# Performance work log

Measured on AMD Instinct MI355X. Metric: run time of the kernel, lower is better.

## Reference

```python
import jax, jax.numpy as jnp
import numpy as np

L, D, B, N, H = 18, 256, 2, 1024, 4
HD = D // H  # head dim = 64
NAMES = ['self', 'cross'] * 9
BN_EPS = 1e-5


def conv1d(x, W, b):
    # pointwise Conv1d: x [B, Cin, N], W [Cout, Cin], b [Cout]
    return jnp.einsum('oi,bin->bon', W, x) + b[None, :, None]


def setup_inputs() -> dict:
    key = jax.random.key(0)
    ks = jax.random.split(key, 20)
    r = lambda k, shp, s=0.02: jax.random.normal(k, shp, dtype=jnp.float32) * s
    inp = {
        'desc0': jax.random.normal(ks[0], (B, D, N), dtype=jnp.float32),
        'desc1': jax.random.normal(ks[1], (B, D, N), dtype=jnp.float32),
        # attention projections (q, k, v, merge), stacked over layers
        'Wq': r(ks[2], (L, D, D)), 'bq': r(ks[3], (L, D)),
        'Wk': r(ks[4], (L, D, D)), 'bk': r(ks[5], (L, D)),
        'Wv': r(ks[6], (L, D, D)), 'bv': r(ks[7], (L, D)),
        'Wm': r(ks[8], (L, D, D)), 'bm': r(ks[9], (L, D)),
        # MLP([2D, 2D, D]): conv1 + BN(eval) + relu + conv2
        'W1': r(ks[10], (L, 2 * D, 2 * D)), 'b1': r(ks[11], (L, 2 * D)),
        'gamma': 1.0 + r(ks[12], (L, 2 * D)), 'beta': r(ks[13], (L, 2 * D)),
        'mu': r(ks[14], (L, 2 * D), 0.1),
        'var': 0.5 + jax.random.uniform(ks[15], (L, 2 * D), dtype=jnp.float32),
        'W2': r(ks[16], (L, D, 2 * D)), 'b2': r(ks[17], (L, D)),
    }
    return inp


def reference(desc0, desc1, Wq, bq, Wk, bk, Wv, bv, Wm, bm,
              W1, b1, gamma, beta, mu, var, W2, b2):
    d0, d1 = desc0, desc1
    bs = d0.shape[0]
    out0, out1 = [], []
    for i, name in enumerate(NAMES):
        x = jnp.concatenate([d0, d1], axis=0)           # [2B, D, N]
        src = x if name == 'self' else jnp.concatenate([d1, d0], axis=0)
        # QKV projections, split D -> (head_dim, H) matching torch .view(B, dim, H, -1)
        q = conv1d(x, Wq[i], bq[i]).reshape(2 * bs, HD, H, N)
        k = conv1d(src, Wk[i], bk[i]).reshape(2 * bs, HD, H, N)
        v = conv1d(src, Wv[i], bv[i]).reshape(2 * bs, HD, H, N)
        scores = jnp.einsum('bdhn,bdhm->bhnm', q, k) / np.sqrt(HD).astype(np.float32)
        prob = jax.nn.softmax(scores, axis=-1)          # [2B, H, N, N]
        att = jnp.einsum('bhnm,bdhm->bdhn', prob, v).reshape(2 * bs, D, N)
        message = conv1d(att, Wm[i], bm[i])             # merge
        y = jnp.concatenate([x, message], axis=1)       # [2B, 2D, N]
        h = conv1d(y, W1[i], b1[i])
        h = gamma[i][None, :, None] * (h - mu[i][None, :, None]) \
            * jax.lax.rsqrt(var[i][None, :, None] + BN_EPS) + beta[i][None, :, None]
        h = jax.nn.relu(h)
        delta = conv1d(h, W2[i], b2[i])                 # [2B, D, N]
        d0 = d0 + delta[:bs]
        d1 = d1 + delta[bs:]
        if name == 'cross':
            out0.append(d0)
            out1.append(d1)
    # [2, n_cross, B, D, N]
    return jnp.stack([jnp.stack(out0), jnp.stack(out1)])
```

## Files before the change

kernel.cpp:

```cpp
#include <hip/hip_runtime.h>
#include <math.h>


typedef unsigned short u16;
typedef unsigned int u32;
typedef __attribute__((ext_vector_type(4))) unsigned int u32x4;
typedef __attribute__((ext_vector_type(2))) unsigned int u32x2;
typedef __attribute__((ext_vector_type(8))) short short8v;
typedef __attribute__((ext_vector_type(4))) float f32x4;

union AB { u32x4 q; u32x2 d[2]; short8v s; };

__device__ __forceinline__ u16 f2bf(float f) {
  u32 u = __builtin_bit_cast(u32, f);
  u32 r = u + 0x7fffu + ((u >> 16) & 1u);
  return (u16)(r >> 16);
}

typedef const __attribute__((address_space(1))) void gas_t;
typedef __attribute__((address_space(3))) void las_t;
__device__ __forceinline__ void gld16(const void* g, void* l) {
  __builtin_amdgcn_global_load_lds((gas_t*)g, (las_t*)l, 16, 0, 0);
}
template<int NN>
__device__ __forceinline__ void waitvm() {
  if constexpr (NN == 0) asm volatile("s_waitcnt vmcnt(0)" ::: "memory");
  else if constexpr (NN == 1) asm volatile("s_waitcnt vmcnt(1)" ::: "memory");
  else asm volatile("s_waitcnt vmcnt(2)" ::: "memory");
}

template<int SN, int NK>
__device__ __forceinline__ void mm16g(const u16* __restrict__ Ar,
                                      const u16* const (&Br)[SN], f32x4 (&acc)[SN]) {
#pragma unroll
  for (int s = 0; s < SN; ++s) acc[s] = (f32x4){0.f, 0.f, 0.f, 0.f};
  AB a[2], b[2][SN];
  a[0].q = *(const u32x4*)(Ar);
#pragma unroll
  for (int s = 0; s < SN; ++s) b[0][s].q = *(const u32x4*)(Br[s]);
#pragma unroll
  for (int kp = 0; kp < NK; ++kp) {
    const int cu = kp & 1, nx = cu ^ 1;
    if (kp + 1 < NK) {
      a[nx].q = *(const u32x4*)(Ar + (kp + 1) * 32);
#pragma unroll
      for (int s = 0; s < SN; ++s) b[nx][s].q = *(const u32x4*)(Br[s] + (kp + 1) * 32);
    }
#pragma unroll
    for (int s = 0; s < SN; ++s)
      acc[s] = __builtin_amdgcn_mfma_f32_16x16x32_bf16(a[cu].s, b[cu][s].s, acc[s], 0, 0, 0);
  }
}

template<int LDB, int SN, int NS, int D>
__device__ __forceinline__ void mmlds(const u16* __restrict__ W, char* __restrict__ Wb,
                                      const char* __restrict__ Alds, f32x4 (&acc)[SN],
                                      int w, int lane, int l4, int l15, int R) {
  constexpr int BUFB = SN * 16384;
  constexpr int NBUF = D + 1;
  const int xj = (lane & 3) ^ ((lane >> 2) & 3) ^ ((lane >> 4) & 3);
  const int swzr = ((l15 & 3) ^ ((l15 >> 2) & 3)) << 4;
  const u16* gs = W + (size_t)(16 * w + (lane >> 2)) * LDB + xj * 8;
  char* ldsu = Wb + 16 * w * 64;
#pragma unroll
  for (int s = 0; s < SN; ++s) acc[s] = (f32x4){0.f, 0.f, 0.f, 0.f};
#pragma unroll
  for (int d = 0; d < D; ++d) {
    const int sl = (R + d) & (NS - 1);
#pragma unroll
    for (int c = 0; c < SN; ++c)
      gld16(gs + (size_t)c * 256 * LDB + (size_t)sl * 32, ldsu + d * BUFB + c * 16384);
  }
#pragma unroll
  for (int i = 0; i < NS; ++i) {
    const int rem = NS - 1 - i;
    if (rem >= D - 1) waitvm<SN*(D - 1)>();
    else if (rem == 1) waitvm<SN>();
    else waitvm<0>();
    __builtin_amdgcn_s_barrier();
    asm volatile("" ::: "memory");
    const int s = (i + R) & (NS - 1);
    const char* rb = Wb + (i % NBUF) * BUFB;
    AB af;
    af.q = *(const u32x4*)(Alds + ((l15 * 1024 + s * 64 + l4 * 16) ^ ((l15 & 7) << 4)));
#pragma unroll
    for (int t = 0; t < SN; ++t) {
      const int col = (w * SN + t) * 16 + l15;
      AB bf;
      bf.q = *(const u32x4*)(rb + col * 64 + ((l4 << 4) ^ swzr));
      acc[t] = __builtin_amdgcn_mfma_f32_16x16x32_bf16(af.s, bf.s, acc[t], 0, 0, 0);
    }
    if (i + D < NS) {
      const int sl = (i + D + R) & (NS - 1);
#pragma unroll
      for (int c = 0; c < SN; ++c)
        gld16(gs + (size_t)c * 256 * LDB + (size_t)sl * 32,
              ldsu + ((i + D) % NBUF) * BUFB + c * 16384);
    }
  }
}

__global__ void k_setup(const float* __restrict__ Wq, const float* __restrict__ Wk,
                        const float* __restrict__ Wv, const float* __restrict__ Wm,
                        const float* __restrict__ W1, const float* __restrict__ W2,
                        const float* __restrict__ g, const float* __restrict__ be,
                        const float* __restrict__ mu, const float* __restrict__ va,
                        const float* __restrict__ b1, u16* __restrict__ wbf,
                        float* __restrict__ sc, float* __restrict__ sh) {
  int bid = blockIdx.x, tid = threadIdx.x;
  if (bid < 4608) {
    int which = bid / 1152, lb = bid - which * 1152;
    size_t i4 = ((size_t)lb * 256 + tid) * 4;
    int layer = (int)(i4 >> 16), rem = (int)(i4 & 65535);
    int row = rem >> 8, kk = rem & 255;
    const float* src = which == 0 ? Wq : which == 1 ? Wk : which == 2 ? Wv : Wm;
    f32x4 a = *(const f32x4*)(src + i4);
    u16* dl = wbf + (size_t)layer * 655360 + which * 65536;
    if (which < 3) {
      float s = (which == 0) ? 0.125f : 1.0f;
      int rp = ((row & 3) << 6) | (row >> 2);
      u32x2 pk;
      pk[0] = (u32)f2bf(a[0] * s) | ((u32)f2bf(a[1] * s) << 16);
      pk[1] = (u32)f2bf(a[2] * s) | ((u32)f2bf(a[3] * s) << 16);
      *(u32x2*)(dl + rp * 256 + kk) = pk;
    } else {
#pragma unroll
      for (int e = 0; e < 4; ++e) {
        int ci = kk + e, cp = ((ci & 3) << 6) | (ci >> 2);
        dl[row * 256 + cp] = f2bf(a[e]);
      }
    }
  } else if (bid < 9216) {
    int lb = bid - 4608;
    size_t i4 = ((size_t)lb * 256 + tid) * 4;
    int layer = (int)(i4 >> 18);
    size_t rem = i4 & 262143;
    f32x4 a = *(const f32x4*)(W1 + i4);
    u32x2 pk;
    pk[0] = (u32)f2bf(a[0]) | ((u32)f2bf(a[1]) << 16);
    pk[1] = (u32)f2bf(a[2]) | ((u32)f2bf(a[3]) << 16);
    *(u32x2*)(wbf + (size_t)layer * 655360 + 262144 + rem) = pk;
  } else if (bid < 11520) {
    int lb = bid - 9216;
    size_t i4 = ((size_t)lb * 256 + tid) * 4;
    int layer = (int)(i4 >> 17);
    size_t rem = i4 & 131071;
    f32x4 a = *(const f32x4*)(W2 + i4);
    u32x2 pk;
    pk[0] = (u32)f2bf(a[0]) | ((u32)f2bf(a[1]) << 16);
    pk[1] = (u32)f2bf(a[2]) | ((u32)f2bf(a[3]) << 16);
    *(u32x2*)(wbf + (size_t)layer * 655360 + 524288 + rem) = pk;
  } else {
    int i = (bid - 11520) * 256 + tid;
    if (i < 9216) {
      float s = g[i] * rsqrtf(va[i] + 1e-5f);
      sc[i] = s;
      sh[i] = s * (b1[i] - mu[i]) + be[i];
    }
  }
}

__global__ __launch_bounds__(256) void k_init(const float* __restrict__ d0,
                                              const float* __restrict__ d1,
                                              float* __restrict__ dstate,
                                              u16* __restrict__ y) {
  __shared__ float T[64 * 65];
  int b = blockIdx.z, cb = blockIdx.y * 64, nb = blockIdx.x * 64;
  int t = threadIdx.x, th = t >> 4, tl = t & 15;
  const float* src = (b < 2 ? d0 : d1) + (size_t)(b & 1) * 262144;
#pragma unroll
  for (int it = 0; it < 4; ++it) {
    int cl = it * 16 + th;
    f32x4 v = *(const f32x4*)(src + (size_t)(cb + cl) * 1024 + nb + tl * 4);
#pragma unroll
    for (int e = 0; e < 4; ++e) T[cl * 65 + tl * 4 + e] = v[e];
  }
  __syncthreads();
#pragma unroll
  for (int it = 0; it < 4; ++it) {
    int nl = it * 16 + th;
    f32x4 o;
#pragma unroll
    for (int e = 0; e < 4; ++e) o[e] = T[(tl * 4 + e) * 65 + nl];
    *(f32x4*)(dstate + (size_t)b * 262144 + (size_t)(nb + nl) * 256 + cb + tl * 4) = o;
    u32x2 pk;
    pk[0] = (u32)f2bf(o[0]) | ((u32)f2bf(o[1]) << 16);
    pk[1] = (u32)f2bf(o[2]) | ((u32)f2bf(o[3]) << 16);
    *(u32x2*)(y + (size_t)b * 524288 + (size_t)(nb + nl) * 512 + cb + tl * 4) = pk;
  }
}

__global__ __launch_bounds__(512) void k_qkv0(const u16* __restrict__ y,
                                              const u16* __restrict__ wln,
                                              const float* __restrict__ bqn,
                                              const float* __restrict__ bkn,
                                              const float* __restrict__ bvn,
                                              u16* __restrict__ qb, u16* __restrict__ kb,
                                              u16* __restrict__ vb) {
  const int row0 = blockIdx.x * 16, b = row0 >> 10, nb0 = row0 & 1023;
  const int tid = threadIdx.x, w = tid >> 6, lane = tid & 63;
  const int l4 = lane >> 4, l15 = lane & 15;
  const u16* Ar = y + (size_t)(row0 + l15) * 512 + l4 * 8;
  const u16* Br[6];
  f32x4 acc[6];
  int ty[6], cc[6];
#pragma unroll
  for (int s = 0; s < 6; ++s) {
    int gc = w * 96 + s * 16;
    ty[s] = gc >> 8;
    cc[s] = gc & 255;
    Br[s] = wln + ty[s] * 65536 + (size_t)(cc[s] + l15) * 256 + l4 * 8;
  }
  mm16g<6, 8>(Ar, Br, acc);
#pragma unroll
  for (int s = 0; s < 6; ++s) {
    int c = cc[s] + l15;
    int borig = ((c & 63) << 2) | (c >> 6);
    if (ty[s] == 0) {
      float bb = 0.125f * bqn[borig];
#pragma unroll
      for (int r = 0; r < 4; ++r)
        qb[(size_t)b * 262144 + (size_t)(nb0 + l4 * 4 + r) * 256 + c] = f2bf(acc[s][r] + bb);
    } else if (ty[s] == 1) {
      float bb = bkn[borig];
#pragma unroll
      for (int r = 0; r < 4; ++r)
        kb[(size_t)b * 262144 + (size_t)(nb0 + l4 * 4 + r) * 256 + c] = f2bf(acc[s][r] + bb);
    } else {
      float bb = bvn[borig];
      u32x2 pk;
      pk[0] = (u32)f2bf(acc[s][0] + bb) | ((u32)f2bf(acc[s][1] + bb) << 16);
      pk[1] = (u32)f2bf(acc[s][2] + bb) | ((u32)f2bf(acc[s][3] + bb) << 16);
      *(u32x2*)(vb + (size_t)b * 262144 + (size_t)c * 1024 + nb0 + l4 * 4) = pk;
    }
  }
}

__global__ __launch_bounds__(512) void k_attn(const u16* __restrict__ qbuf,
                                              const u16* __restrict__ kbuf,
                                              const u16* __restrict__ vbuf,
                                              u16* __restrict__ att, int crossmask) {
  __shared__ char Kt[2][2][8192];
  __shared__ char Vt[2][2][8192];
  __shared__ char Ps[8][2304];
  __shared__ float Ms[4][16], Ls[4][16], Os[4][16][68];
  const int nb = blockIdx.x * 64;
  const int bh = blockIdx.y, b = bh >> 2, h = bh & 3;
  const int srcb = b ^ crossmask;
  const int tid = threadIdx.x, w = tid >> 6, lane = tid & 63;
  const int l4 = lane >> 4, l15 = lane & 15;
  const int qt = w & 3, half = w >> 2;
  char* P = Ps[w];
  const u16* Qb = qbuf + (size_t)b * 262144 + h * 64;
  const u16* Kb = kbuf + (size_t)srcb * 262144 + h * 64;
  const u16* Vb = vbuf + (size_t)srcb * 262144 + (size_t)h * 65536;
  const int srow = tid >> 3, sj = (tid & 7) * 16, sx = sj ^ ((srow & 7) << 4);
  const u16* gK[2] = {Kb, Kb + 512 * 256};
  const u16* gV[2] = {Vb, Vb + 512};

  const int qrow = nb + qt * 16;
  AB qf[2];
#pragma unroll
  for (int ks = 0; ks < 2; ++ks)
    qf[ks].q = *(const u32x4*)(Qb + (size_t)(qrow + l15) * 256 + ks * 32 + l4 * 8);

  u32x4 sk[2], sv[2];
#pragma unroll
  for (int H = 0; H < 2; ++H) {
    sk[H] = *(const u32x4*)((const char*)(gK[H] + (size_t)srow * 256) + sj);
    sv[H] = *(const u32x4*)((const char*)(gV[H] + (size_t)srow * 1024) + sj);
  }
#pragma unroll
  for (int H = 0; H < 2; ++H) {
    *(u32x4*)(Kt[H][0] + srow * 128 + sx) = sk[H];
    *(u32x4*)(Vt[H][0] + srow * 128 + sx) = sv[H];
  }
  __syncthreads();

  f32x4 oacc[4];
#pragma unroll
  for (int s = 0; s < 4; ++s) oacc[s] = (f32x4){0.f, 0.f, 0.f, 0.f};
  float mst = -1e30f, lst = 0.f;

#pragma unroll
  for (int mt = 0; mt < 8; ++mt) {
    const int cur = mt & 1, nx = cur ^ 1;
    if (mt < 7) {
#pragma unroll
      for (int H = 0; H < 2; ++H) {
        sk[H] = *(const u32x4*)((const char*)(gK[H] + (size_t)((mt + 1) * 64 + srow) * 256) + sj);
        sv[H] = *(const u32x4*)((const char*)(gV[H] + (size_t)srow * 1024 + (mt + 1) * 64) + sj);
      }
    }
    f32x4 sa[4];
#pragma unroll
    for (int sm = 0; sm < 4; ++sm) {
      sa[sm] = (f32x4){0.f, 0.f, 0.f, 0.f};
#pragma unroll
      for (int ks = 0; ks < 2; ++ks) {
        AB kf;
        int rr = sm * 16 + l15;
        kf.q = *(const u32x4*)(Kt[half][cur] + rr * 128 + ((ks * 64 + l4 * 16) ^ ((rr & 7) << 4)));
        sa[sm] = __builtin_amdgcn_mfma_f32_16x16x32_bf16(kf.s, qf[ks].s, sa[sm], 0, 0, 0);
      }
    }
    float m1 = fmaxf(fmaxf(fmaxf(sa[0][0], sa[0][1]), fmaxf(sa[0][2], sa[0][3])),
                     fmaxf(fmaxf(sa[1][0], sa[1][1]), fmaxf(sa[1][2], sa[1][3])));
    float m2 = fmaxf(fmaxf(fmaxf(sa[2][0], sa[2][1]), fmaxf(sa[2][2], sa[2][3])),
                     fmaxf(fmaxf(sa[3][0], sa[3][1]), fmaxf(sa[3][2], sa[3][3])));
    m1 = fmaxf(m1, m2);
    m1 = fmaxf(m1, __shfl_xor(m1, 16));
    m1 = fmaxf(m1, __shfl_xor(m1, 32));
    float mnew = fmaxf(mst, m1);
    float corr = __expf(mst - mnew);
    mst = mnew;
    float rs = 0.f;
#pragma unroll
    for (int sm = 0; sm < 4; ++sm)
#pragma unroll
      for (int r = 0; r < 4; ++r) {
        float p = __expf(sa[sm][r] - mnew);
        sa[sm][r] = p;
        rs += p;
      }
    rs += __shfl_xor(rs, 16);
    rs += __shfl_xor(rs, 32);
    lst = lst * corr + rs;
#pragma unroll
    for (int r = 0; r < 4; ++r) {
      float cr = __shfl(corr, l4 * 4 + r);
#pragma unroll
      for (int s = 0; s < 4; ++s) oacc[s][r] *= cr;
    }
#pragma unroll
    for (int sm = 0; sm < 4; ++sm) {
      u32x2 pk;
      pk[0] = (u32)f2bf(sa[sm][0]) | ((u32)f2bf(sa[sm][1]) << 16);
      pk[1] = (u32)f2bf(sa[sm][2]) | ((u32)f2bf(sa[sm][3]) << 16);
      *(u32x2*)(P + l15 * 136 + (sm * 16 + l4 * 4) * 2) = pk;
    }
#pragma unroll
    for (int ks = 0; ks < 2; ++ks) {
      AB pf;
      const char* ra = P + l15 * 136 + ks * 64 + l4 * 16;
      pf.d[0] = *(const u32x2*)ra;
      pf.d[1] = *(const u32x2*)(ra + 8);
#pragma unroll
      for (int s = 0; s < 4; ++s) {
        AB vf;
        int rr = s * 16 + l15;
        vf.q = *(const u32x4*)(Vt[half][cur] + rr * 128 + ((ks * 64 + l4 * 16) ^ ((rr & 7) << 4)));
        oacc[s] = __builtin_amdgcn_mfma_f32_16x16x32_bf16(pf.s, vf.s, oacc[s], 0, 0, 0);
      }
    }
    if (mt < 7) {
#pragma unroll
      for (int H = 0; H < 2; ++H) {
        *(u32x4*)(Kt[H][nx] + srow * 128 + sx) = sk[H];
        *(u32x4*)(Vt[H][nx] + srow * 128 + sx) = sv[H];
      }
    }
    __syncthreads();
  }
  if (half == 1) {
    Ms[qt][l15] = mst;
    Ls[qt][l15] = lst;
#pragma unroll
    for (int s = 0; s < 4; ++s)
#pragma unroll
      for (int r = 0; r < 4; ++r) Os[qt][l4 * 4 + r][s * 16 + l15] = oacc[s][r];
  }
  __syncthreads();
  if (half == 0) {
    float mb = Ms[qt][l15], lb = Ls[qt][l15];
    float M = fmaxf(mst, mb);
    float ea = __expf(mst - M), eb = __expf(mb - M);
    float rl = 1.f / (lst * ea + lb * eb);
    float fa = ea * rl, fb = eb * rl;
#pragma unroll
    for (int r = 0; r < 4; ++r) {
      float far = __shfl(fa, l4 * 4 + r);
      float fbr = __shfl(fb, l4 * 4 + r);
      int n = nb + qt * 16 + l4 * 4 + r;
#pragma unroll
      for (int s = 0; s < 4; ++s) {
        float ov = oacc[s][r] * far + Os[qt][l4 * 4 + r][s * 16 + l15] * fbr;
        att[(size_t)b * 262144 + (size_t)n * 256 + h * 64 + s * 16 + l15] = f2bf(ov);
      }
    }
  }
}

__global__ __launch_bounds__(1024) void k_post(
    const u16* __restrict__ att, const u16* __restrict__ wl, const u16* __restrict__ wln,
    const float* __restrict__ bm, const float* __restrict__ sc, const float* __restrict__ sh,
    const float* __restrict__ b2, const float* __restrict__ bqn,
    const float* __restrict__ bkn, const float* __restrict__ bvn,
    float* __restrict__ dstate, u16* __restrict__ y, u16* __restrict__ qb,
    u16* __restrict__ kb, u16* __restrict__ vb, float* __restrict__ out, int cross, int j,
    int last) {
  __shared__ char yT[16384];
  __shared__ char hT[16384];
  __shared__ char Wb[98304];
  const int bid = blockIdx.x;
  const int row0 = bid * 16, b = row0 >> 10, nb0 = row0 & 1023;
  const int tid = threadIdx.x, w = tid >> 6, lane = tid & 63;
  const int l4 = lane >> 4, l15 = lane & 15;

  {
    int rr = tid >> 6, ch = tid & 63;
    u32x4 v = *(const u32x4*)(y + (size_t)(row0 + rr) * 512 + ch * 8);
    *(u32x4*)(yT + ((rr * 1024 + ch * 16) ^ ((rr & 7) << 4))) = v;
    if (tid < 512) {
      int ra = tid >> 5, ca = tid & 31;
      u32x4 va = *(const u32x4*)(att + (size_t)(row0 + ra) * 256 + ca * 8);
      *(u32x4*)(hT + ((ra * 1024 + ca * 16) ^ ((ra & 7) << 4))) = va;
    }
  }
  __syncthreads();
  {
    f32x4 acc[1];
    mmlds<256, 1, 8, 3>(wl + 196608, Wb, hT, acc, w, lane, l4, l15, bid & 7);
    int c = w * 16 + l15;
    float bb = bm[c];
#pragma unroll
    for (int r = 0; r < 4; ++r) {
      int rw = l4 * 4 + r;
      *(u16*)(yT + ((rw * 1024 + (256 + c) * 2) ^ ((rw & 7) << 4))) = f2bf(acc[0][r] + bb);
    }
  }
  __syncthreads();
  {
    f32x4 acc[2];
    mmlds<512, 2, 16, 2>(wl + 262144, Wb, yT, acc, w, lane, l4, l15, bid & 15);
#pragma unroll
    for (int s = 0; s < 2; ++s) {
      int c = w * 32 + s * 16 + l15;
      float s_ = sc[c], t_ = sh[c];
#pragma unroll
      for (int r = 0; r < 4; ++r) {
        int rw = l4 * 4 + r;
        *(u16*)(hT + ((rw * 1024 + c * 2) ^ ((rw & 7) << 4))) =
            f2bf(fmaxf(s_ * acc[s][r] + t_, 0.f));
      }
    }
  }
  __syncthreads();
  {
    f32x4 acc[1];
    mmlds<512, 1, 16, 3>(wl + 524288, Wb, hT, acc, w, lane, l4, l15, bid & 15);
    float* ob = out + (size_t)(((b >> 1) * 9 + j) * 2 + (b & 1)) * 262144;
    int c = w * 16 + l15;
    float bb = b2[c];
#pragma unroll
    for (int r = 0; r < 4; ++r) {
      int rw = l4 * 4 + r;
      size_t di = (size_t)(row0 + rw) * 256 + c;
      float nv = dstate[di] + acc[0][r] + bb;
      dstate[di] = nv;
      u16 bv16 = f2bf(nv);
      y[(size_t)(row0 + rw) * 512 + c] = bv16;
      *(u16*)(yT + ((rw * 1024 + c * 2) ^ ((rw & 7) << 4))) = bv16;
      if (cross) ob[(size_t)c * 1024 + nb0 + rw] = nv;
    }
  }
  if (last) return;
  __syncthreads();
  {
    f32x4 acc[2];
    mmlds<256, 2, 8, 2>(wln, Wb, yT, acc, w, lane, l4, l15, bid & 7);
#pragma unroll
    for (int s = 0; s < 2; ++s) {
      int gc = w * 32 + s * 16;
      int ty = gc >> 8;
      int c = (gc & 255) + l15;
      int borig = ((c & 63) << 2) | (c >> 6);
      if (ty == 0) {
        float bb = 0.125f * bqn[borig];
#pragma unroll
        for (int r = 0; r < 4; ++r)
          qb[(size_t)b * 262144 + (size_t)(nb0 + l4 * 4 + r) * 256 + c] = f2bf(acc[s][r] + bb);
      } else {
        float bb = bkn[borig];
#pragma unroll
        for (int r = 0; r < 4; ++r)
          kb[(size_t)b * 262144 + (size_t)(nb0 + l4 * 4 + r) * 256 + c] = f2bf(acc[s][r] + bb);
      }
    }
  }
  __syncthreads();
  {
    f32x4 acc[1];
    mmlds<256, 1, 8, 3>(wln + 131072, Wb, yT, acc, w, lane, l4, l15, bid & 7);
    int c = w * 16 + l15;
    float bb = bvn[((c & 63) << 2) | (c >> 6)];
    u32x2 pk;
    pk[0] = (u32)f2bf(acc[0][0] + bb) | ((u32)f2bf(acc[0][1] + bb) << 16);
    pk[1] = (u32)f2bf(acc[0][2] + bb) | ((u32)f2bf(acc[0][3] + bb) << 16);
    *(u32x2*)(vb + (size_t)b * 262144 + (size_t)c * 1024 + nb0 + l4 * 4) = pk;
  }
}

extern "C" void kernel_launch(void* const* d_in, const int* in_sizes, int n_in,
                              void* d_out, int out_size, void* d_ws, size_t ws_size,
                              hipStream_t stream) {
  const float* desc0 = (const float*)d_in[0];
  const float* desc1 = (const float*)d_in[1];
  const float* Wq = (const float*)d_in[2];
  const float* bq = (const float*)d_in[3];
  const float* Wk = (const float*)d_in[4];
  const float* bk = (const float*)d_in[5];
  const float* Wv = (const float*)d_in[6];
  const float* bv = (const float*)d_in[7];
  const float* Wm = (const float*)d_in[8];
  const float* bm = (const float*)d_in[9];
  const float* W1 = (const float*)d_in[10];
  const float* b1 = (const float*)d_in[11];
  const float* gamma = (const float*)d_in[12];
  const float* beta = (const float*)d_in[13];
  const float* mu = (const float*)d_in[14];
  const float* var = (const float*)d_in[15];
  const float* W2 = (const float*)d_in[16];
  const float* b2 = (const float*)d_in[17];

  char* ws = (char*)d_ws;
  float* dstate = (float*)ws;
  u16* y = (u16*)(ws + ((size_t)4 << 20));
  u16* qb = (u16*)(ws + ((size_t)8 << 20));
  u16* kb = (u16*)(ws + ((size_t)10 << 20));
  u16* vb = (u16*)(ws + ((size_t)12 << 20));
  u16* attb = (u16*)(ws + ((size_t)14 << 20));
  u16* wbf = (u16*)(ws + ((size_t)16 << 20));
  float* scb = (float*)(ws + ((size_t)40 << 20));
  float* shb = (float*)(ws + ((size_t)41 << 20));

  k_setup<<<11556, 256, 0, stream>>>(Wq, Wk, Wv, Wm, W1, W2, gamma, beta, mu, var, b1,
                                     wbf, scb, shb);
  k_init<<<dim3(16, 4, 4), 256, 0, stream>>>(desc0, desc1, dstate, y);
  k_qkv0<<<256, 512, 0, stream>>>(y, wbf, bq, bk, bv, qb, kb, vb);

  for (int i = 0; i < 18; ++i) {
    int cross = i & 1;
    const u16* wl = wbf + (size_t)i * 655360;
    int nl = (i < 17) ? i + 1 : 0;
    const u16* wln = wbf + (size_t)nl * 655360;
    k_attn<<<dim3(16, 16), 512, 0, stream>>>(qb, kb, vb, attb, cross ? 2 : 0);
    k_post<<<256, 1024, 0, stream>>>(attb, wl, wln, bm + i * 256, scb + (size_t)i * 512,
                                     shb + (size_t)i * 512, b2 + i * 256, bq + nl * 256,
                                     bk + nl * 256, bv + nl * 256, dstate, y, qb, kb, vb,
                                     (float*)d_out, cross, i >> 1, i == 17);
  }
}
```

Before: 778.2 us.

## Double k_post row tile and give each wave a private weight ring

k_post now handles 32 rows per block instead of 16, with half as many blocks, so each weight slice streamed from global memory feeds two MFMA row groups. The shared, barrier-synchronised weight staging buffer is replaced by a per-wave three-slot ring, and each wave loads only its own 16-column slice, so the per-step block barriers go away. The cost is that only 128 blocks remain to occupy the GPU, and each wave now issues more sequential weight passes, which may expose load latency.

```diff
diff --git a/kernel.cpp b/kernel.cpp
--- a/kernel.cpp
+++ b/kernel.cpp
@@ -25,8 +25,7 @@
 template<int NN>
 __device__ __forceinline__ void waitvm() {
   if constexpr (NN == 0) asm volatile("s_waitcnt vmcnt(0)" ::: "memory");
-  else if constexpr (NN == 1) asm volatile("s_waitcnt vmcnt(1)" ::: "memory");
-  else asm volatile("s_waitcnt vmcnt(2)" ::: "memory");
+  else asm volatile("s_waitcnt vmcnt(1)" ::: "memory");
 }
 
 template<int SN, int NK>
@@ -52,50 +51,35 @@
   }
 }
 
-template<int LDB, int SN, int NS, int D>
-__device__ __forceinline__ void mmlds(const u16* __restrict__ W, char* __restrict__ Wb,
-                                      const char* __restrict__ Alds, f32x4 (&acc)[SN],
-                                      int w, int lane, int l4, int l15, int R) {
-  constexpr int BUFB = SN * 16384;
-  constexpr int NBUF = D + 1;
+template<int LDB, int NS>
+__device__ __forceinline__ void mmw(const u16* __restrict__ Wcol, char* __restrict__ ldsw,
+                                    const char* __restrict__ Alds, f32x4 (&acc)[2],
+                                    int lane, int l4, int l15, int R) {
   const int xj = (lane & 3) ^ ((lane >> 2) & 3) ^ ((lane >> 4) & 3);
   const int swzr = ((l15 & 3) ^ ((l15 >> 2) & 3)) << 4;
-  const u16* gs = W + (size_t)(16 * w + (lane >> 2)) * LDB + xj * 8;
-  char* ldsu = Wb + 16 * w * 64;
-#pragma unroll
-  for (int s = 0; s < SN; ++s) acc[s] = (f32x4){0.f, 0.f, 0.f, 0.f};
-#pragma unroll
-  for (int d = 0; d < D; ++d) {
+  const u16* gs = Wcol + (size_t)(lane >> 2) * LDB + xj * 8;
+  acc[0] = (f32x4){0.f, 0.f, 0.f, 0.f};
+  acc[1] = (f32x4){0.f, 0.f, 0.f, 0.f};
+#pragma unroll
+  for (int d = 0; d < 2; ++d) {
     const int sl = (R + d) & (NS - 1);
-#pragma unroll
-    for (int c = 0; c < SN; ++c)
-      gld16(gs + (size_t)c * 256 * LDB + (size_t)sl * 32, ldsu + d * BUFB + c * 16384);
+    gld16(gs + (size_t)sl * 32, ldsw + d * 1024);
   }
 #pragma unroll
   for (int i = 0; i < NS; ++i) {
-    const int rem = NS - 1 - i;
-    if (rem >= D - 1) waitvm<SN*(D - 1)>();
-    else if (rem == 1) waitvm<SN>();
+    if (i < NS - 1) waitvm<1>();
     else waitvm<0>();
-    __builtin_amdgcn_s_barrier();
-    asm volatile("" ::: "memory");
     const int s = (i + R) & (NS - 1);
-    const char* rb = Wb + (i % NBUF) * BUFB;
-    AB af;
-    af.q = *(const u32x4*)(Alds + ((l15 * 1024 + s * 64 + l4 * 16) ^ ((l15 & 7) << 4)));
-#pragma unroll
-    for (int t = 0; t < SN; ++t) {
-      const int col = (w * SN + t) * 16 + l15;
-      AB bf;
-      bf.q = *(const u32x4*)(rb + col * 64 + ((l4 << 4) ^ swzr));
-      acc[t] = __builtin_amdgcn_mfma_f32_16x16x32_bf16(af.s, bf.s, acc[t], 0, 0, 0);
-    }
-    if (i + D < NS) {
-      const int sl = (i + D + R) & (NS - 1);
-#pragma unroll
-      for (int c = 0; c < SN; ++c)
-        gld16(gs + (size_t)c * 256 * LDB + (size_t)sl * 32,
-              ldsu + ((i + D) % NBUF) * BUFB + c * 16384);
+    const char* rb = ldsw + (i % 3) * 1024;
+    AB af0, af1, bf;
+    af0.q = *(const u32x4*)(Alds + ((l15 * 1024 + s * 64 + l4 * 16) ^ ((l15 & 7) << 4)));
+    af1.q = *(const u32x4*)(Alds + (((16 + l15) * 1024 + s * 64 + l4 * 16) ^ ((l15 & 7) << 4)));
+    bf.q = *(const u32x4*)(rb + l15 * 64 + ((l4 << 4) ^ swzr));
+    acc[0] = __builtin_amdgcn_mfma_f32_16x16x32_bf16(af0.s, bf.s, acc[0], 0, 0, 0);
+    acc[1] = __builtin_amdgcn_mfma_f32_16x16x32_bf16(af1.s, bf.s, acc[1], 0, 0, 0);
+    if (i + 2 < NS) {
+      const int sl = (i + 2 + R) & (NS - 1);
+      gld16(gs + (size_t)sl * 32, ldsw + ((i + 2) % 3) * 1024);
     }
   }
 }
@@ -399,19 +383,24 @@
     float* __restrict__ dstate, u16* __restrict__ y, u16* __restrict__ qb,
     u16* __restrict__ kb, u16* __restrict__ vb, float* __restrict__ out, int cross, int j,
     int last) {
-  __shared__ char yT[16384];
-  __shared__ char hT[16384];
-  __shared__ char Wb[98304];
+  __shared__ char yT[32768];
+  __shared__ char hT[32768];
+  __shared__ char Wb[49152];
   const int bid = blockIdx.x;
-  const int row0 = bid * 16, b = row0 >> 10, nb0 = row0 & 1023;
+  const int row0 = bid * 32, b = row0 >> 10, nb0 = row0 & 1023;
   const int tid = threadIdx.x, w = tid >> 6, lane = tid & 63;
   const int l4 = lane >> 4, l15 = lane & 15;
+  char* ring = Wb + w * 3072;
 
   {
-    int rr = tid >> 6, ch = tid & 63;
-    u32x4 v = *(const u32x4*)(y + (size_t)(row0 + rr) * 512 + ch * 8);
-    *(u32x4*)(yT + ((rr * 1024 + ch * 16) ^ ((rr & 7) << 4))) = v;
-    if (tid < 512) {
+#pragma unroll
+    for (int it = 0; it < 2; ++it) {
+      int idx = it * 1024 + tid;
+      int rr = idx >> 6, ch = idx & 63;
+      u32x4 v = *(const u32x4*)(y + (size_t)(row0 + rr) * 512 + ch * 8);
+      *(u32x4*)(yT + ((rr * 1024 + ch * 16) ^ ((rr & 7) << 4))) = v;
+    }
+    {
       int ra = tid >> 5, ca = tid & 31;
       u32x4 va = *(const u32x4*)(att + (size_t)(row0 + ra) * 256 + ca * 8);
       *(u32x4*)(hT + ((ra * 1024 + ca * 16) ^ ((ra & 7) << 4))) = va;
@@ -419,85 +408,97 @@
   }
   __syncthreads();
   {
-    f32x4 acc[1];
-    mmlds<256, 1, 8, 3>(wl + 196608, Wb, hT, acc, w, lane, l4, l15, bid & 7);
+    f32x4 acc[2];
+    mmw<256, 8>(wl + 196608 + (size_t)(w * 16) * 256, ring, hT, acc, lane, l4, l15, bid & 7);
     int c = w * 16 + l15;
     float bb = bm[c];
 #pragma unroll
-    for (int r = 0; r < 4; ++r) {
-      int rw = l4 * 4 + r;
-      *(u16*)(yT + ((rw * 1024 + (256 + c) * 2) ^ ((rw & 7) << 4))) = f2bf(acc[0][r] + bb);
+    for (int g = 0; g < 2; ++g)
+#pragma unroll
+      for (int r = 0; r < 4; ++r) {
+        int rw = g * 16 + l4 * 4 + r;
+        *(u16*)(yT + ((rw * 1024 + (256 + c) * 2) ^ ((rw & 7) << 4))) = f2bf(acc[g][r] + bb);
+      }
+  }
+  __syncthreads();
+  {
+#pragma unroll
+    for (int p = 0; p < 2; ++p) {
+      f32x4 acc[2];
+      const int colbase = p * 256 + w * 16;
+      mmw<512, 16>(wl + 262144 + (size_t)colbase * 512, ring, yT, acc, lane, l4, l15,
+                   (bid + p * 5) & 15);
+      int c = colbase + l15;
+      float s_ = sc[c], t_ = sh[c];
+#pragma unroll
+      for (int g = 0; g < 2; ++g)
+#pragma unroll
+        for (int r = 0; r < 4; ++r) {
+          int rw = g * 16 + l4 * 4 + r;
+          *(u16*)(hT + ((rw * 1024 + c * 2) ^ ((rw & 7) << 4))) =
+              f2bf(fmaxf(s_ * acc[g][r] + t_, 0.f));
+        }
     }
   }
   __syncthreads();
   {
     f32x4 acc[2];
-    mmlds<512, 2, 16, 2>(wl + 262144, Wb, yT, acc, w, lane, l4, l15, bid & 15);
-#pragma unroll
-    for (int s = 0; s < 2; ++s) {
-      int c = w * 32 + s * 16 + l15;
-      float s_ = sc[c], t_ = sh[c];
-#pragma unroll
-      for (int r = 0; r < 4; ++r) {
-        int rw = l4 * 4 + r;
-        *(u16*)(hT + ((rw * 1024 + c * 2) ^ ((rw & 7) << 4))) =
-            f2bf(fmaxf(s_ * acc[s][r] + t_, 0.f));
-      }
-    }
-  }
-  __syncthreads();
-  {
-    f32x4 acc[1];
-    mmlds<512, 1, 16, 3>(wl + 524288, Wb, hT, acc, w, lane, l4, l15, bid & 15);
+    mmw<512, 16>(wl + 524288 + (size_t)(w * 16) * 512, ring, hT, acc, lane, l4, l15,
+                 bid & 15);
     float* ob = out + (size_t)(((b >> 1) * 9 + j) * 2 + (b & 1)) * 262144;
     int c = w * 16 + l15;
     float bb = b2[c];
 #pragma unroll
-    for (int r = 0; r < 4; ++r) {
-      int rw = l4 * 4 + r;
-      size_t di = (size_t)(row0 + rw) * 256 + c;
-      float nv = dstate[di] + acc[0][r] + bb;
-      dstate[di] = nv;
-      u16 bv16 = f2bf(nv);
-      y[(size_t)(row0 + rw) * 512 + c] = bv16;
-      *(u16*)(yT + ((rw * 1024 + c * 2) ^ ((rw & 7) << 4))) = bv16;
-      if (cross) ob[(size_t)c * 1024 + nb0 + rw] = nv;
-    }
+    for (int g = 0; g < 2; ++g)
+#pragma unroll
+      for (int r = 0; r < 4; ++r) {
+        int rw = g * 16 + l4 * 4 + r;
+        size_t di = (size_t)(row0 + rw) * 256 + c;
+        float nv = dstate[di] + acc[g][r] + bb;
+        dstate[di] = nv;
+        u16 bv16 = f2bf(nv);
+        y[(size_t)(row0 + rw) * 512 + c] = bv16;
+        *(u16*)(yT + ((rw * 1024 + c * 2) ^ ((rw & 7) << 4))) = bv16;
+        if (cross) ob[(size_t)c * 1024 + nb0 + rw] = nv;
+      }
   }
   if (last) return;
   __syncthreads();
   {
-    f32x4 acc[2];
-    mmlds<256, 2, 8, 2>(wln, Wb, yT, acc, w, lane, l4, l15, bid & 7);
-#pragma unroll
-    for (int s = 0; s < 2; ++s) {
-      int gc = w * 32 + s * 16;
-      int ty = gc >> 8;
-      int c = (gc & 255) + l15;
+#pragma unroll
+    for (int p = 0; p < 3; ++p) {
+      f32x4 acc[2];
+      mmw<256, 8>(wln + p * 65536 + (size_t)(w * 16) * 256, ring, yT, acc, lane, l4, l15,
+                  (bid + p * 3) & 7);
+      int c = w * 16 + l15;
       int borig = ((c & 63) << 2) | (c >> 6);
-      if (ty == 0) {
+      if (p == 0) {
         float bb = 0.125f * bqn[borig];
 #pragma unroll
-        for (int r = 0; r < 4; ++r)
-          qb[(size_t)b * 262144 + (size_t)(nb0 + l4 * 4 + r) * 256 + c] = f2bf(acc[s][r] + bb);
+        for (int g = 0; g < 2; ++g)
+#pragma unroll
+          for (int r = 0; r < 4; ++r)
+            qb[(size_t)b * 262144 + (size_t)(nb0 + g * 16 + l4 * 4 + r) * 256 + c] =
+                f2bf(acc[g][r] + bb);
+      } else if (p == 1) {
+        float bb = bkn[borig];
+#pragma unroll
+        for (int g = 0; g < 2; ++g)
+#pragma unroll
+          for (int r = 0; r < 4; ++r)
+            kb[(size_t)b * 262144 + (size_t)(nb0 + g * 16 + l4 * 4 + r) * 256 + c] =
+                f2bf(acc[g][r] + bb);
       } else {
-        float bb = bkn[borig];
-#pragma unroll
-        for (int r = 0; r < 4; ++r)
-          kb[(size_t)b * 262144 + (size_t)(nb0 + l4 * 4 + r) * 256 + c] = f2bf(acc[s][r] + bb);
-      }
-    }
-  }
-  __syncthreads();
-  {
-    f32x4 acc[1];
-    mmlds<256, 1, 8, 3>(wln + 131072, Wb, yT, acc, w, lane, l4, l15, bid & 7);
-    int c = w * 16 + l15;
-    float bb = bvn[((c & 63) << 2) | (c >> 6)];
-    u32x2 pk;
-    pk[0] = (u32)f2bf(acc[0][0] + bb) | ((u32)f2bf(acc[0][1] + bb) << 16);
-    pk[1] = (u32)f2bf(acc[0][2] + bb) | ((u32)f2bf(acc[0][3] + bb) << 16);
-    *(u32x2*)(vb + (size_t)b * 262144 + (size_t)c * 1024 + nb0 + l4 * 4) = pk;
+        float bb = bvn[borig];
+#pragma unroll
+        for (int g = 0; g < 2; ++g) {
+          u32x2 pk;
+          pk[0] = (u32)f2bf(acc[g][0] + bb) | ((u32)f2bf(acc[g][1] + bb) << 16);
+          pk[1] = (u32)f2bf(acc[g][2] + bb) | ((u32)f2bf(acc[g][3] + bb) << 16);
+          *(u32x2*)(vb + (size_t)b * 262144 + (size_t)c * 1024 + nb0 + g * 16 + l4 * 4) = pk;
+        }
+      }
+    }
   }
 }
 
@@ -545,7 +546,7 @@
     int nl = (i < 17) ? i + 1 : 0;
     const u16* wln = wbf + (size_t)nl * 655360;
     k_attn<<<dim3(16, 16), 512, 0, stream>>>(qb, kb, vb, attb, cross ? 2 : 0);
-    k_post<<<256, 1024, 0, stream>>>(attb, wl, wln, bm + i * 256, scb + (size_t)i * 512,
+    k_post<<<128, 1024, 0, stream>>>(attb, wl, wln, bm + i * 256, scb + (size_t)i * 512,
                                      shb + (size_t)i * 512, b2 + i * 256, bq + nl * 256,
                                      bk + nl * 256, bv + nl * 256, dstate, y, qb, kb, vb,
                                      (float*)d_out, cross, i >> 1, i == 17);
```

Result: no change. 775.3 us (-0.4%).
